# Performance work log

Measured on AMD Instinct MI355X. Metric: run time of the kernel, lower is better.

## Reference

```python
import jax, jax.numpy as jnp
import numpy as np

B, N, D = 8, 2048, 512
H, DH = 8, 64
SCALE = DH ** -0.5


def setup_inputs() -> dict:
    key = jax.random.key(0)
    ks = jax.random.split(key, 7)
    x = jax.random.normal(ks[0], (B, N, D), dtype=jnp.float32)
    mask = jax.random.uniform(ks[1], (B, N, N), dtype=jnp.float32)
    Wq = jax.random.normal(ks[2], (D, H * DH), dtype=jnp.float32) * (D ** -0.5)
    Wk = jax.random.normal(ks[3], (D, H * DH), dtype=jnp.float32) * (D ** -0.5)
    Wv = jax.random.normal(ks[4], (D, H * DH), dtype=jnp.float32) * (D ** -0.5)
    Wo = jax.random.normal(ks[5], (H * DH, D), dtype=jnp.float32) * ((H * DH) ** -0.5)
    bo = jnp.zeros((D,), dtype=jnp.float32)
    return {"x": x, "mask": mask, "Wq": Wq, "Wk": Wk, "Wv": Wv, "Wo": Wo, "bo": bo}


def reference(x, mask, Wq, Wk, Wv, Wo, bo):
    b, n, d = x.shape
    # QKV projections -> [b, h, n, dh]
    q = (x @ Wq).reshape(b, n, H, DH).transpose(0, 2, 1, 3)
    k = (x @ Wk).reshape(b, n, H, DH).transpose(0, 2, 1, 3)
    v = (x @ Wv).reshape(b, n, H, DH).transpose(0, 2, 1, 3)
    # scores with multiplicative structural mask bias: dots * (1 + M)
    dots = jnp.einsum('bhid,bhjd->bhij', q, k) * SCALE
    dots = dots * (1.0 + mask[:, None, :, :])
    attn = jax.nn.softmax(dots, axis=-1)  # dropout is identity in eval
    out = jnp.einsum('bhij,bhjd->bhid', attn, v)
    out = out.transpose(0, 2, 1, 3).reshape(b, n, H * DH)
    return out @ Wo + bo
```

## Files before the change

### kernel.cpp

```cpp
#include <hip/hip_runtime.h>

typedef __bf16 bf16;
typedef __bf16 bf16x8 __attribute__((ext_vector_type(8)));
typedef float  f32x4  __attribute__((ext_vector_type(4)));
typedef unsigned u32x4 __attribute__((ext_vector_type(4)));

#define B_  8
#define N_  2048
#define D_  512
#define H_  8
#define DH_ 64
static constexpr float SC2 = 0.18033688011112042f;

#if defined(__has_builtin)
#if __has_builtin(__builtin_amdgcn_exp2f)
#define EXP2(x) __builtin_amdgcn_exp2f(x)
#else
#define EXP2(x) exp2f(x)
#endif
#else
#define EXP2(x) exp2f(x)
#endif

#if defined(__has_builtin)
#if __has_builtin(__builtin_amdgcn_permlane32_swap) && __has_builtin(__builtin_amdgcn_permlane16_swap)
#define HAVE_PLSWAP 1
#endif
#endif

__device__ __forceinline__ f32x4 mfma16(bf16x8 a, bf16x8 b, f32x4 c) {
  return __builtin_amdgcn_mfma_f32_16x16x32_bf16(a, b, c, 0, 0, 0);
}

__device__ __forceinline__ void gload_lds16(const void* g, void* l) {
  __builtin_amdgcn_global_load_lds((__attribute__((address_space(1))) void*)g,
                                   (__attribute__((address_space(3))) void*)l, 16, 0, 0);
}

__device__ __forceinline__ unsigned cvt_pk_bf16(float lo, float hi) {
  unsigned r;
  asm("v_cvt_pk_bf16_f32 %0, %1, %2" : "=v"(r) : "v"(lo), "v"(hi));
  return r;
}

__global__ void k_cvt_x(const float* __restrict__ x, bf16* __restrict__ xb) {
  int i = blockIdx.x * blockDim.x + threadIdx.x;
  const float4* p = (const float4*)x;
  float4 a = p[2*i], b = p[2*i+1];
  bf16x8 o;
  o[0]=(bf16)a.x; o[1]=(bf16)a.y; o[2]=(bf16)a.z; o[3]=(bf16)a.w;
  o[4]=(bf16)b.x; o[5]=(bf16)b.y; o[6]=(bf16)b.z; o[7]=(bf16)b.w;
  ((bf16x8*)xb)[i] = o;
}

__global__ void k_wt(const float* __restrict__ w, bf16* __restrict__ wt) {
  __shared__ float t[64][65];
  const int c0 = blockIdx.x * 64, k0 = blockIdx.y * 64;
  const int r = threadIdx.x >> 2, q4 = (threadIdx.x & 3) * 16;
#pragma unroll
  for (int j = 0; j < 16; j += 4) {
    float4 v = *(const float4*)(w + (k0 + r) * 512 + c0 + q4 + j);
    t[r][q4+j] = v.x; t[r][q4+j+1] = v.y; t[r][q4+j+2] = v.z; t[r][q4+j+3] = v.w;
  }
  __syncthreads();
  const int c = threadIdx.x >> 2, kq = (threadIdx.x & 3) * 16;
  bf16x8 o0, o1;
#pragma unroll
  for (int j = 0; j < 8; ++j) { o0[j] = (bf16)t[kq+j][c]; o1[j] = (bf16)t[kq+8+j][c]; }
  *(bf16x8*)(wt + (c0 + c) * 512 + k0 + kq) = o0;
  *(bf16x8*)(wt + (c0 + c) * 512 + k0 + kq + 8) = o1;
}

template<int MODE>
__global__ void k_gemm(const bf16* __restrict__ A, const bf16* __restrict__ Bt,
                       bf16* __restrict__ qo, bf16* __restrict__ ko, bf16* __restrict__ vo,
                       float* __restrict__ outp, const float* __restrict__ bo) {
  __shared__ bf16 lA[128 * 64];
  __shared__ bf16 lB[128 * 64];
  const int tid = threadIdx.x;
  const int wid = tid >> 6, lane = tid & 63;
  const int l15 = lane & 15, lq = lane >> 4;
  const int wr = wid >> 1, wc = wid & 1;
  const long long rowtile = (long long)blockIdx.x * 128;
  const long long coltile = (long long)blockIdx.y * 128;

  const bf16* gA[4]; const bf16* gB[4];
  bf16* lAc[4]; bf16* lBc[4];
#pragma unroll
  for (int i = 0; i < 4; ++i) {
    int ci = wid * 4 + i;
    int row = ci * 8 + (lane >> 3);
    int c8 = (lane & 7) ^ (row & 7);
    gA[i] = A + (rowtile + row) * 512 + c8 * 8;
    gB[i] = Bt + (coltile + row) * 512 + c8 * 8;
    lAc[i] = &lA[ci * 512];
    lBc[i] = &lB[ci * 512];
  }
  unsigned aoff[4][2], boff[4][2];
#pragma unroll
  for (int mi = 0; mi < 4; ++mi) {
#pragma unroll
    for (int ks = 0; ks < 2; ++ks) {
      int R = l15 + 16 * mi + 64 * wr;
      aoff[mi][ks] = R * 128 + ((((ks << 2) | lq) ^ (R & 7)) << 4);
      int Rb = l15 + 16 * mi + 64 * wc;
      boff[mi][ks] = Rb * 128 + ((((ks << 2) | lq) ^ (Rb & 7)) << 4);
    }
  }
  f32x4 acc[4][4] = {};
  for (int kt = 0; kt < 8; ++kt) {
#pragma unroll
    for (int i = 0; i < 4; ++i) gload_lds16(gA[i], lAc[i]);
#pragma unroll
    for (int i = 0; i < 4; ++i) gload_lds16(gB[i], lBc[i]);
#pragma unroll
    for (int i = 0; i < 4; ++i) { gA[i] += 64; gB[i] += 64; }
    __syncthreads();
#pragma unroll
    for (int ks = 0; ks < 2; ++ks) {
      bf16x8 af[4], bfr[4];
#pragma unroll
      for (int mi = 0; mi < 4; ++mi) af[mi] = *(const bf16x8*)((const char*)lA + aoff[mi][ks]);
#pragma unroll
      for (int nf = 0; nf < 4; ++nf) bfr[nf] = *(const bf16x8*)((const char*)lB + boff[nf][ks]);
#pragma unroll
      for (int mi = 0; mi < 4; ++mi)
#pragma unroll
        for (int nf = 0; nf < 4; ++nf)
          acc[mi][nf] = mfma16(af[mi], bfr[nf], acc[mi][nf]);
    }
    __syncthreads();
  }
  if (MODE == 0) {
#pragma unroll
    for (int nf = 0; nf < 4; ++nf) {
      const int col = (int)coltile + 64 * wc + nf * 16 + l15;
      const int mat = col >> 9, c5 = col & 511, hh = c5 >> 6, dh = c5 & 63;
#pragma unroll
      for (int mi = 0; mi < 4; ++mi) {
#pragma unroll
        for (int r = 0; r < 4; ++r) {
          const int R = (int)rowtile + 64 * wr + mi * 16 + lq * 4 + r;
          const int bb = R >> 11, n = R & 2047;
          const bf16 bv = (bf16)acc[mi][nf][r];
          const long long bh = bb * 8 + hh;
          if (mat == 0)      qo[(bh * 2048 + n) * 64 + dh] = bv;
          else if (mat == 1) ko[(bh * 2048 + n) * 64 + dh] = bv;
          else               vo[(bh * 64 + dh) * 2048 + n] = bv;
        }
      }
    }
  } else {
#pragma unroll
    for (int nf = 0; nf < 4; ++nf) {
      const int col = (int)coltile + 64 * wc + nf * 16 + l15;
      const float bias = bo[col];
#pragma unroll
      for (int mi = 0; mi < 4; ++mi)
#pragma unroll
        for (int r = 0; r < 4; ++r) {
          const long long R = rowtile + 64 * wr + mi * 16 + lq * 4 + r;
          outp[R * 512 + col] = acc[mi][nf][r] + bias;
        }
    }
  }
}

__global__ __launch_bounds__(256, 3) void k_attn(
    const bf16* __restrict__ qb, const bf16* __restrict__ kb, const bf16* __restrict__ vt,
    const float* __restrict__ mask, bf16* __restrict__ ao) {
  __shared__ __align__(16) bf16 kvls[2][2][64 * 64];
  const int tid = threadIdx.x;
  const int lane = tid & 63;
  const int wid = tid >> 6;
  const int l15 = lane & 15, lq = lane >> 4;
  const int p = blockIdx.x;
  const int xcd = p & 7, kk = p >> 3;
  const int g = xcd * 16 + (kk >> 3), h = kk & 7;
  const int b = g >> 4, qt = g & 15;
  const long long bh = b * 8 + h;
  const bf16* Q = qb + bh * (2048ll * 64);
  const bf16* K = kb + bh * (2048ll * 64);
  const bf16* V = vt + bh * (64ll * 2048);
  const int qrow0 = qt * 128 + wid * 32;
  const float* mptr0 = mask + ((long long)b * 2048 + qrow0 + l15) * 2048 + lq * 4;
  const float* mptr1 = mptr0 + 16 * 2048;

  const int row0 = tid >> 3, row1 = row0 + 32;
  const int sc = (tid & 7) ^ (row0 & 7);
  const bf16* kg0 = K + row0 * 64 + sc * 8;
  const bf16* vg0 = V + row0 * 2048 + sc * 8;
  const bf16* vg1 = V + row1 * 2048 + sc * 8;

  bf16x8 qf[2][2];
#pragma unroll
  for (int mi = 0; mi < 2; ++mi)
#pragma unroll
    for (int ks = 0; ks < 2; ++ks)
      qf[mi][ks] = *(const bf16x8*)(Q + (qrow0 + mi * 16 + l15) * 64 + ks * 32 + lq * 8);

  f32x4 o[2][4] = {};
  float lsum0 = 0.f, lsum1 = 0.f;
  f32x4 mA[4], mB[4];

  auto stageKV = [&](int buf, int jt) {
    gload_lds16(kg0 + jt * 4096,        &kvls[buf][0][tid * 8]);
    gload_lds16(kg0 + jt * 4096 + 2048, &kvls[buf][0][tid * 8 + 2048]);
    gload_lds16(vg0 + jt * 64,          &kvls[buf][1][tid * 8]);
    gload_lds16(vg1 + jt * 64,          &kvls[buf][1][tid * 8 + 2048]);
  };

  auto smax = [&](f32x4 (&m)[4], const float* mp, const f32x4 (&sm)[4], float& ls,
                  bf16x8& pA, bf16x8& pB, bool pref, int jbn) {
    unsigned w[4][2];
#pragma unroll
    for (int nf = 0; nf < 4; ++nf) {
      float mp0 = fmaf(m[nf][0], SC2, SC2);
      float mp1 = fmaf(m[nf][1], SC2, SC2);
      float mp2 = fmaf(m[nf][2], SC2, SC2);
      float mp3 = fmaf(m[nf][3], SC2, SC2);
      float pe0 = EXP2(sm[nf][0] * mp0);
      float pe1 = EXP2(sm[nf][1] * mp1);
      float pe2 = EXP2(sm[nf][2] * mp2);
      float pe3 = EXP2(sm[nf][3] * mp3);
      ls += ((pe0 + pe1) + (pe2 + pe3));
      w[nf][0] = cvt_pk_bf16(pe0, pe1);
      w[nf][1] = cvt_pk_bf16(pe2, pe3);
    }
    if (pref) {
#pragma unroll
      for (int nf = 0; nf < 4; ++nf)
        m[nf] = *(const f32x4*)(mp + jbn + nf * 16);
    }
    unsigned pa0[4], pa1[4];
#ifdef HAVE_PLSWAP
#pragma unroll
    for (int t = 0; t < 2; ++t) {
      auto sA = __builtin_amdgcn_permlane32_swap(w[0][t], w[1][t], false, false);
      auto sB = __builtin_amdgcn_permlane16_swap(sA[0], sA[1], false, false);
      pa0[t] = sB[0]; pa0[t + 2] = sB[1];
      auto sC = __builtin_amdgcn_permlane32_swap(w[2][t], w[3][t], false, false);
      auto sD = __builtin_amdgcn_permlane16_swap(sC[0], sC[1], false, false);
      pa1[t] = sD[0]; pa1[t + 2] = sD[1];
    }
#else
    {
      const int basel = l15 + ((lq & 1) << 5);
#pragma unroll
      for (int t = 0; t < 2; ++t) {
        int sel0 = (lq & 2) ? (int)w[1][t] : (int)w[0][t];
        int sel1 = (lq & 2) ? (int)w[3][t] : (int)w[2][t];
        pa0[t]     = (unsigned)__shfl(sel0, basel);
        pa0[t + 2] = (unsigned)__shfl(sel0, basel + 16);
        pa1[t]     = (unsigned)__shfl(sel1, basel);
        pa1[t + 2] = (unsigned)__shfl(sel1, basel + 16);
      }
    }
#endif
    u32x4 ua = {pa0[0], pa0[1], pa0[2], pa0[3]};
    u32x4 ub = {pa1[0], pa1[1], pa1[2], pa1[3]};
    pA = __builtin_bit_cast(bf16x8, ua);
    pB = __builtin_bit_cast(bf16x8, ub);
  };

  stageKV(0, 0);
#pragma unroll
  for (int nf = 0; nf < 4; ++nf) {
    mA[nf] = *(const f32x4*)(mptr0 + nf * 16);
    mB[nf] = *(const f32x4*)(mptr1 + nf * 16);
  }
  __syncthreads();

  for (int jt = 0; jt < 32; ++jt) {
    const int buf = jt & 1;
    const bool morejt = (jt + 1 < 32);
    if (morejt) stageKV(buf ^ 1, jt + 1);
    const bf16* kbL = &kvls[buf][0][0];
    const bf16* vbL = &kvls[buf][1][0];

    f32x4 s[2][4];
    {
      bf16x8 kf0[4], kf1[4];
#pragma unroll
      for (int nf = 0; nf < 4; ++nf) {
        const int row = nf * 16 + l15;
        kf0[nf] = *(const bf16x8*)(kbL + row * 64 + ((lq ^ (row & 7)) << 3));
        kf1[nf] = *(const bf16x8*)(kbL + row * 64 + (((4 + lq) ^ (row & 7)) << 3));
      }
#pragma unroll
      for (int mi = 0; mi < 2; ++mi)
#pragma unroll
        for (int nf = 0; nf < 4; ++nf) {
          f32x4 z = {0.f, 0.f, 0.f, 0.f};
          s[mi][nf] = mfma16(kf0[nf], qf[mi][0], z);
        }
#pragma unroll
      for (int mi = 0; mi < 2; ++mi)
#pragma unroll
        for (int nf = 0; nf < 4; ++nf)
          s[mi][nf] = mfma16(kf1[nf], qf[mi][1], s[mi][nf]);
    }

    bf16x8 paA0, paB0, paA1, paB1;
    smax(mA, mptr0, s[0], lsum0, paA0, paB0, morejt, (jt + 1) * 64);
    smax(mB, mptr1, s[1], lsum1, paA1, paB1, morejt, (jt + 1) * 64);

#pragma unroll
    for (int nf = 0; nf < 4; ++nf) {
      const int row = nf * 16 + l15;
      const bf16x8 vf = *(const bf16x8*)(vbL + row * 64 + ((lq ^ (row & 7)) << 3));
      o[0][nf] = mfma16(paA0, vf, o[0][nf]);
      o[1][nf] = mfma16(paA1, vf, o[1][nf]);
    }
#pragma unroll
    for (int nf = 0; nf < 4; ++nf) {
      const int row = nf * 16 + l15;
      const bf16x8 vf = *(const bf16x8*)(vbL + row * 64 + (((4 + lq) ^ (row & 7)) << 3));
      o[0][nf] = mfma16(paB0, vf, o[0][nf]);
      o[1][nf] = mfma16(paB1, vf, o[1][nf]);
    }
    __syncthreads();
  }

  float v0 = lsum0, v1 = lsum1;
  v0 += __shfl_xor(v0, 16); v0 += __shfl_xor(v0, 32);
  v1 += __shfl_xor(v1, 16); v1 += __shfl_xor(v1, 32);
  const float ri0 = 1.0f / v0, ri1 = 1.0f / v1;
  float rv[2][4];
#pragma unroll
  for (int r = 0; r < 4; ++r) {
    rv[0][r] = __shfl(ri0, ((lane & 48) >> 2) + r);
    rv[1][r] = __shfl(ri1, ((lane & 48) >> 2) + r);
  }
#pragma unroll
  for (int mi = 0; mi < 2; ++mi)
#pragma unroll
    for (int nf = 0; nf < 4; ++nf)
#pragma unroll
      for (int r = 0; r < 4; ++r) {
        const long long rowg = (long long)b * 2048 + qrow0 + mi * 16 + lq * 4 + r;
        ao[rowg * 512 + h * 64 + nf * 16 + l15] = (bf16)(o[mi][nf][r] * rv[mi][r]);
      }
}

extern "C" void kernel_launch(void* const* d_in, const int* in_sizes, int n_in,
                              void* d_out, int out_size, void* d_ws, size_t ws_size,
                              hipStream_t stream) {
  const float* x    = (const float*)d_in[0];
  const float* mask = (const float*)d_in[1];
  const float* Wq   = (const float*)d_in[2];
  const float* Wk   = (const float*)d_in[3];
  const float* Wv   = (const float*)d_in[4];
  const float* Wo   = (const float*)d_in[5];
  const float* bo   = (const float*)d_in[6];
  float* out = (float*)d_out;
  char* ws = (char*)d_ws;

  const size_t SZ_XB = (size_t)16384 * 512 * 2;
  const size_t SZ_W3 = (size_t)1536 * 512 * 2;
  const size_t SZ_WO = (size_t)512 * 512 * 2;
  const size_t SZ_T  = (size_t)64 * 2048 * 64 * 2;

  bf16* xb    = (bf16*)ws;
  bf16* wqkvT = (bf16*)(ws + SZ_XB);
  bf16* woT   = (bf16*)(ws + SZ_XB + SZ_W3);
  bf16* qbuf  = (bf16*)(ws + SZ_XB + SZ_W3 + SZ_WO);
  bf16* kbuf  = (bf16*)((char*)qbuf + SZ_T);
  bf16* vtb   = (bf16*)((char*)kbuf + SZ_T);
  bf16* aob   = xb;

  k_cvt_x<<<dim3(4096), dim3(256), 0, stream>>>(x, xb);
  k_wt<<<dim3(8, 8), dim3(256), 0, stream>>>(Wq, wqkvT);
  k_wt<<<dim3(8, 8), dim3(256), 0, stream>>>(Wk, wqkvT + 512 * 512);
  k_wt<<<dim3(8, 8), dim3(256), 0, stream>>>(Wv, wqkvT + 2 * 512 * 512);
  k_wt<<<dim3(8, 8), dim3(256), 0, stream>>>(Wo, woT);
  k_gemm<0><<<dim3(128, 12), dim3(256), 0, stream>>>(xb, wqkvT, qbuf, kbuf, vtb, nullptr, nullptr);
  k_attn<<<dim3(1024), dim3(256), 0, stream>>>(qbuf, kbuf, vtb, mask, aob);
  k_gemm<1><<<dim3(128, 4), dim3(256), 0, stream>>>(aob, woT, nullptr, nullptr, nullptr, out, bo);
}
```

Baseline: 256.1 us.

## Hand-schedule LDS reads with inline asm and issue V reads before softmax

Replaces the compiler-generated K and V fragment loads from LDS with inline ds_read_b128 using precomputed swizzled base addresses and immediate offsets. The V fragment reads are issued before the softmax so their LDS latency is hidden behind the exp work, with explicit lgkmcnt waits and sched barriers. The mask loads for each tile now happen inside the loop for the current tile instead of being prefetched one tile ahead, which may expose global load latency. Inline asm and sched barriers limit the compiler's freedom to reorder instructions.

```diff
diff --git a/kernel.cpp b/kernel.cpp
--- a/kernel.cpp
+++ b/kernel.cpp
@@ -42,6 +42,9 @@
   asm("v_cvt_pk_bf16_f32 %0, %1, %2" : "=v"(r) : "v"(lo), "v"(hi));
   return r;
 }
+
+#define DSR(dst, a, off) \
+  asm volatile("ds_read_b128 %0, %1 offset:" off : "=v"(dst) : "v"(a))
 
 __global__ void k_cvt_x(const float* __restrict__ x, bf16* __restrict__ xb) {
   int i = blockIdx.x * blockDim.x + threadIdx.x;
@@ -186,11 +189,15 @@
   const float* mptr0 = mask + ((long long)b * 2048 + qrow0 + l15) * 2048 + lq * 4;
   const float* mptr1 = mptr0 + 16 * 2048;
 
-  const int row0 = tid >> 3, row1 = row0 + 32;
+  const int row0 = tid >> 3;
   const int sc = (tid & 7) ^ (row0 & 7);
   const bf16* kg0 = K + row0 * 64 + sc * 8;
   const bf16* vg0 = V + row0 * 2048 + sc * 8;
-  const bf16* vg1 = V + row1 * 2048 + sc * 8;
+  const bf16* vg1 = V + (row0 + 32) * 2048 + sc * 8;
+
+  const unsigned lbase = (unsigned)(size_t)(&kvls[0][0][0]) + (unsigned)(l15 * 128);
+  const unsigned aks0 = lbase + (((unsigned)(lq ^ (l15 & 7))) << 4);
+  const unsigned aks1 = lbase + (((unsigned)((4 + lq) ^ (l15 & 7))) << 4);
 
   bf16x8 qf[2][2];
 #pragma unroll
@@ -201,7 +208,6 @@
 
   f32x4 o[2][4] = {};
   float lsum0 = 0.f, lsum1 = 0.f;
-  f32x4 mA[4], mB[4];
 
   auto stageKV = [&](int buf, int jt) {
     gload_lds16(kg0 + jt * 4096,        &kvls[buf][0][tid * 8]);
@@ -210,8 +216,8 @@
     gload_lds16(vg1 + jt * 64,          &kvls[buf][1][tid * 8 + 2048]);
   };
 
-  auto smax = [&](f32x4 (&m)[4], const float* mp, const f32x4 (&sm)[4], float& ls,
-                  bf16x8& pA, bf16x8& pB, bool pref, int jbn) {
+  auto smax = [&](const f32x4 (&m)[4], const f32x4 (&sm)[4], float& ls,
+                  bf16x8& pA, bf16x8& pB) {
     unsigned w[4][2];
 #pragma unroll
     for (int nf = 0; nf < 4; ++nf) {
@@ -227,11 +233,6 @@
       w[nf][0] = cvt_pk_bf16(pe0, pe1);
       w[nf][1] = cvt_pk_bf16(pe2, pe3);
     }
-    if (pref) {
-#pragma unroll
-      for (int nf = 0; nf < 4; ++nf)
-        m[nf] = *(const f32x4*)(mp + jbn + nf * 16);
-    }
     unsigned pa0[4], pa1[4];
 #ifdef HAVE_PLSWAP
 #pragma unroll
@@ -264,68 +265,83 @@
   };
 
   stageKV(0, 0);
-#pragma unroll
-  for (int nf = 0; nf < 4; ++nf) {
-    mA[nf] = *(const f32x4*)(mptr0 + nf * 16);
-    mB[nf] = *(const f32x4*)(mptr1 + nf * 16);
-  }
   __syncthreads();
 
   for (int jt = 0; jt < 32; ++jt) {
     const int buf = jt & 1;
-    const bool morejt = (jt + 1 < 32);
-    if (morejt) stageKV(buf ^ 1, jt + 1);
-    const bf16* kbL = &kvls[buf][0][0];
-    const bf16* vbL = &kvls[buf][1][0];
+    if (jt + 1 < 32) stageKV(buf ^ 1, jt + 1);
+
+    f32x4 mA[4], mB[4];
+    const int jb = jt * 64;
+#pragma unroll
+    for (int nf = 0; nf < 4; ++nf) {
+      mA[nf] = *(const f32x4*)(mptr0 + jb + nf * 16);
+      mB[nf] = *(const f32x4*)(mptr1 + jb + nf * 16);
+    }
+
+    const unsigned bo4 = (unsigned)(buf << 14);
+    const unsigned k0a = aks0 + bo4, k1a = aks1 + bo4;
+
+    f32x4 t0, t1, t2, t3, t4, t5, t6, t7;
+    DSR(t0, k0a, "0");    DSR(t1, k0a, "2048");
+    DSR(t2, k0a, "4096"); DSR(t3, k0a, "6144");
+    DSR(t4, k1a, "0");    DSR(t5, k1a, "2048");
+    DSR(t6, k1a, "4096"); DSR(t7, k1a, "6144");
+    asm volatile("s_waitcnt lgkmcnt(0)" ::: "memory");
+    __builtin_amdgcn_sched_barrier(0);
+    bf16x8 kf0[4] = { __builtin_bit_cast(bf16x8, t0), __builtin_bit_cast(bf16x8, t1),
+                      __builtin_bit_cast(bf16x8, t2), __builtin_bit_cast(bf16x8, t3) };
+    bf16x8 kf1[4] = { __builtin_bit_cast(bf16x8, t4), __builtin_bit_cast(bf16x8, t5),
+                      __builtin_bit_cast(bf16x8, t6), __builtin_bit_cast(bf16x8, t7) };
 
     f32x4 s[2][4];
-    {
-      bf16x8 kf0[4], kf1[4];
+#pragma unroll
+    for (int mi = 0; mi < 2; ++mi)
 #pragma unroll
       for (int nf = 0; nf < 4; ++nf) {
-        const int row = nf * 16 + l15;
-        kf0[nf] = *(const bf16x8*)(kbL + row * 64 + ((lq ^ (row & 7)) << 3));
-        kf1[nf] = *(const bf16x8*)(kbL + row * 64 + (((4 + lq) ^ (row & 7)) << 3));
+        f32x4 z = {0.f, 0.f, 0.f, 0.f};
+        s[mi][nf] = mfma16(kf0[nf], qf[mi][0], z);
       }
 #pragma unroll
-      for (int mi = 0; mi < 2; ++mi)
-#pragma unroll
-        for (int nf = 0; nf < 4; ++nf) {
-          f32x4 z = {0.f, 0.f, 0.f, 0.f};
-          s[mi][nf] = mfma16(kf0[nf], qf[mi][0], z);
-        }
-#pragma unroll
-      for (int mi = 0; mi < 2; ++mi)
-#pragma unroll
-        for (int nf = 0; nf < 4; ++nf)
-          s[mi][nf] = mfma16(kf1[nf], qf[mi][1], s[mi][nf]);
-    }
+    for (int mi = 0; mi < 2; ++mi)
+#pragma unroll
+      for (int nf = 0; nf < 4; ++nf)
+        s[mi][nf] = mfma16(kf1[nf], qf[mi][1], s[mi][nf]);
+
+    f32x4 v0, v1, v2, v3, v4, v5, v6, v7;
+    DSR(v0, k0a, "8192");  DSR(v1, k0a, "10240");
+    DSR(v2, k0a, "12288"); DSR(v3, k0a, "14336");
+    DSR(v4, k1a, "8192");  DSR(v5, k1a, "10240");
+    DSR(v6, k1a, "12288"); DSR(v7, k1a, "14336");
 
     bf16x8 paA0, paB0, paA1, paB1;
-    smax(mA, mptr0, s[0], lsum0, paA0, paB0, morejt, (jt + 1) * 64);
-    smax(mB, mptr1, s[1], lsum1, paA1, paB1, morejt, (jt + 1) * 64);
-
-#pragma unroll
-    for (int nf = 0; nf < 4; ++nf) {
-      const int row = nf * 16 + l15;
-      const bf16x8 vf = *(const bf16x8*)(vbL + row * 64 + ((lq ^ (row & 7)) << 3));
-      o[0][nf] = mfma16(paA0, vf, o[0][nf]);
-      o[1][nf] = mfma16(paA1, vf, o[1][nf]);
-    }
-#pragma unroll
-    for (int nf = 0; nf < 4; ++nf) {
-      const int row = nf * 16 + l15;
-      const bf16x8 vf = *(const bf16x8*)(vbL + row * 64 + (((4 + lq) ^ (row & 7)) << 3));
-      o[0][nf] = mfma16(paB0, vf, o[0][nf]);
-      o[1][nf] = mfma16(paB1, vf, o[1][nf]);
+    smax(mA, s[0], lsum0, paA0, paB0);
+    smax(mB, s[1], lsum1, paA1, paB1);
+
+    asm volatile("s_waitcnt lgkmcnt(0)" ::: "memory");
+    __builtin_amdgcn_sched_barrier(0);
+    bf16x8 vf0[4] = { __builtin_bit_cast(bf16x8, v0), __builtin_bit_cast(bf16x8, v1),
+                      __builtin_bit_cast(bf16x8, v2), __builtin_bit_cast(bf16x8, v3) };
+    bf16x8 vf1[4] = { __builtin_bit_cast(bf16x8, v4), __builtin_bit_cast(bf16x8, v5),
+                      __builtin_bit_cast(bf16x8, v6), __builtin_bit_cast(bf16x8, v7) };
+
+#pragma unroll
+    for (int nf = 0; nf < 4; ++nf) {
+      o[0][nf] = mfma16(paA0, vf0[nf], o[0][nf]);
+      o[1][nf] = mfma16(paA1, vf0[nf], o[1][nf]);
+    }
+#pragma unroll
+    for (int nf = 0; nf < 4; ++nf) {
+      o[0][nf] = mfma16(paB0, vf1[nf], o[0][nf]);
+      o[1][nf] = mfma16(paB1, vf1[nf], o[1][nf]);
     }
     __syncthreads();
   }
 
-  float v0 = lsum0, v1 = lsum1;
-  v0 += __shfl_xor(v0, 16); v0 += __shfl_xor(v0, 32);
-  v1 += __shfl_xor(v1, 16); v1 += __shfl_xor(v1, 32);
-  const float ri0 = 1.0f / v0, ri1 = 1.0f / v1;
+  float va = lsum0, vb = lsum1;
+  va += __shfl_xor(va, 16); va += __shfl_xor(va, 32);
+  vb += __shfl_xor(vb, 16); vb += __shfl_xor(vb, 32);
+  const float ri0 = 1.0f / va, ri1 = 1.0f / vb;
   float rv[2][4];
 #pragma unroll
   for (int r = 0; r < 4; ++r) {
```

After: 252.4 us. Within noise of the previous version (-1.4%).
